# Kernel optimization log

Measured on AMD Instinct MI355X. Metric: run time of the kernel, lower is better.

Reference implementation:

```python
import jax, jax.numpy as jnp
import numpy as np

INPUT_SIZE = 1
HIDDEN = 20


def setup_inputs() -> dict:
    key = jax.random.key(0)
    ks = jax.random.split(key, 7)
    B, S = 4096, 512
    scale = 1.0 / np.sqrt(HIDDEN)  # torch LSTM/Linear init range
    x = jax.random.normal(ks[0], (B, S, INPUT_SIZE), dtype=jnp.float32)
    W_ih = jax.random.uniform(ks[1], (4 * HIDDEN, INPUT_SIZE), jnp.float32, -scale, scale)
    W_hh = jax.random.uniform(ks[2], (4 * HIDDEN, HIDDEN), jnp.float32, -scale, scale)
    b_ih = jax.random.uniform(ks[3], (4 * HIDDEN,), jnp.float32, -scale, scale)
    b_hh = jax.random.uniform(ks[4], (4 * HIDDEN,), jnp.float32, -scale, scale)
    W_lin = jax.random.uniform(ks[5], (1, HIDDEN), jnp.float32, -scale, scale)
    b_lin = jax.random.uniform(ks[6], (1,), jnp.float32, -scale, scale)
    return {"x": x, "W_ih": W_ih, "W_hh": W_hh, "b_ih": b_ih,
            "b_hh": b_hh, "W_lin": W_lin, "b_lin": b_lin}


def _lstm_seq(x, W_ih, W_hh, b_ih, b_hh):
    # x: [B, S, 1]; returns all hidden states [B, S, H]
    B = x.shape[0]
    # precompute input contribution for all timesteps: [S, B, 4H]
    xg = jnp.einsum('bsi,gi->sbg', x, W_ih) + (b_ih + b_hh)
    h0 = jnp.zeros((B, HIDDEN), x.dtype)
    c0 = jnp.zeros((B, HIDDEN), x.dtype)

    def step(carry, xg_t):
        h, c = carry
        gates = xg_t + h @ W_hh.T  # [B, 4H]
        i, f, g, o = jnp.split(gates, 4, axis=-1)  # torch gate order: i,f,g,o
        i = jax.nn.sigmoid(i)
        f = jax.nn.sigmoid(f)
        g = jnp.tanh(g)
        o = jax.nn.sigmoid(o)
        c_new = f * c + i * g
        h_new = o * jnp.tanh(c_new)
        return (h_new, c_new), h_new

    _, hs = jax.lax.scan(step, (h0, c0), xg)  # hs: [S, B, H]
    return jnp.transpose(hs, (1, 0, 2))  # [B, S, H]


def reference(x, W_ih, W_hh, b_ih, b_hh, W_lin, b_lin):
    h = _lstm_seq(x, W_ih, W_hh, b_ih, b_hh)  # [B, S, H]
    return h @ W_lin.T + b_lin  # [B, S, 1]
```

## Files before the change

kernel.cpp:

```cpp
#include <hip/hip_runtime.h>


#define BATCH 4096
#define SLEN  512
#define H     20
#define LOG2E 1.44269504088896340736f

typedef _Float16 f16x8 __attribute__((ext_vector_type(8)));
typedef _Float16 h2    __attribute__((ext_vector_type(2)));
typedef float    f32x4 __attribute__((ext_vector_type(4)));

__device__ __forceinline__ float fexp2(float x) { return __builtin_amdgcn_exp2f(x); }
__device__ __forceinline__ float frcp(float x)  { return __builtin_amdgcn_rcpf(x); }

#define ACT(Cv, CC, HV) {                                             \
    const float eI = fexp2((Cv)[0]);                                  \
    const float eF = fexp2((Cv)[1]);                                  \
    const float eG = fexp2((Cv)[2]);                                  \
    const float eO = fexp2((Cv)[3]);                                  \
    const float pF = 1.0f + eF;                                       \
    const float P  = (1.0f + eI) * (1.0f + eG);                       \
    const float num = fmaf(CC, P, (1.0f - eG) * pF);                  \
    CC = fmaxf(num * frcp(pF * P), -34.0f);                           \
    const float eC = fexp2(s2 * CC);                                  \
    HV = (1.0f - eC) * frcp((1.0f + eO) * (1.0f + eC));               \
}

__global__ __launch_bounds__(256, 1) void lstm_fused(
    const float* __restrict__ x,
    const float* __restrict__ W_ih,
    const float* __restrict__ W_hh,
    const float* __restrict__ b_ih,
    const float* __restrict__ b_hh,
    const float* __restrict__ W_lin,
    const float* __restrict__ b_lin,
    float* __restrict__ out)
{
    __shared__ __align__(16) _Float16 hrow[2][16][40];

    const int tid  = threadIdx.x;
    const int wv   = tid >> 6;
    const int lane = tid & 63;
    const int q    = lane >> 4;
    const int n    = lane & 15;
    const long b   = (long)blockIdx.x * 16 + n;

    const float s1 = -LOG2E;
    const float s2 = -2.0f * LOG2E;

    const int  m0   = (wv == 0) ? 0 : (wv + 1);
    const bool dual = (wv == 0);

    const int gA = n & 3;
    const int uA = (n >> 2) * 5;
    const float scA = (gA == 2) ? s2 : s1;
    f16x8 am0, am1;
    {
        const int r0 = gA * H + uA + m0;
        const int r1 = gA * H + uA + 1;
#pragma unroll
        for (int s = 0; s < 8; ++s) {
            am0[s] = (_Float16)((s < 5) ? scA * W_hh[r0 * H + 5 * q + s] : 0.0f);
            am1[s] = (_Float16)((s < 5) ? scA * W_hh[r1 * H + 5 * q + s] : 0.0f);
        }
    }
    f16x8 ah;
#pragma unroll
    for (int s = 0; s < 8; ++s)
        ah[s] = (_Float16)((n == 0 && s < 5) ? W_lin[5 * q + s] : 0.0f);
    const f32x4 chi = {(q == 0) ? b_lin[0] : 0.0f, 0.0f, 0.0f, 0.0f};

    f32x4 xw0, bb0, xw1, bb1;
#pragma unroll
    for (int r = 0; r < 4; ++r) {
        const float sc = (r == 2) ? s2 : s1;
        const int r0 = r * H + 5 * q + m0;
        const int r1 = r * H + 5 * q + 1;
        xw0[r] = sc * W_ih[r0];  bb0[r] = sc * (b_ih[r0] + b_hh[r0]);
        xw1[r] = sc * W_ih[r1];  bb1[r] = sc * (b_ih[r1] + b_hh[r1]);
    }

    const float* xb = x + b * SLEN;
    float*       ob = out + b * SLEN;

    for (int i = tid; i < 640; i += 256) ((unsigned*)hrow)[i] = 0u;
    __syncthreads();

    float cc0 = 0.0f, cc1 = 0.0f;
    f32x4 ya;
    f32x4 xc = *(const f32x4*)xb;

#define STEP(p)                                                            \
    {                                                                      \
        const f16x8 bf = *(const f16x8*)&hrow[((p) & 1) ^ 1][n][8 * q];    \
        if (wv == 3) {                                                     \
            const f32x4 Ch =                                               \
                __builtin_amdgcn_mfma_f32_16x16x32_f16(ah, bf, chi, 0, 0, 0); \
            const float yv = Ch[0];                  \
            if ((p) == 0) {                                                \
                ya[3] = yv;                                                \
                if (k > 0 && lane < 16) *(f32x4*)(ob + 4 * k - 4) = ya;    \
            } else if ((p) == 1) ya[0] = yv;                               \
            else if ((p) == 2) ya[1] = yv;                                 \
            else ya[2] = yv;                                               \
        }                                                                  \
        const float xt = xc[(p)];                                          \
        f32x4 ci0;                                                         \
        ci0[0] = fmaf(xt, xw0[0], bb0[0]);                                 \
        ci0[1] = fmaf(xt, xw0[1], bb0[1]);                                 \
        ci0[2] = fmaf(xt, xw0[2], bb0[2]);                                 \
        ci0[3] = fmaf(xt, xw0[3], bb0[3]);                                 \
        f32x4 C0 = __builtin_amdgcn_mfma_f32_16x16x32_f16(am0, bf, ci0, 0, 0, 0); \
        float h0v;                                                         \
        ACT(C0, cc0, h0v);                                                 \
        if (dual) {                                                        \
            f32x4 ci1;                                                     \
            ci1[0] = fmaf(xt, xw1[0], bb1[0]);                             \
            ci1[1] = fmaf(xt, xw1[1], bb1[1]);                             \
            ci1[2] = fmaf(xt, xw1[2], bb1[2]);                             \
            ci1[3] = fmaf(xt, xw1[3], bb1[3]);                             \
            f32x4 C1 = __builtin_amdgcn_mfma_f32_16x16x32_f16(am1, bf, ci1, 0, 0, 0); \
            float h1v;                                                     \
            ACT(C1, cc1, h1v);                                             \
            h2 pr; pr.x = (_Float16)h0v; pr.y = (_Float16)h1v;             \
            *(h2*)&hrow[(p) & 1][n][8 * q] = pr;          \
        } else {                                                           \
            hrow[(p) & 1][n][8 * q + m0] = (_Float16)h0v;                  \
        }                                                                  \
        __syncthreads();                                                   \
    }

#pragma unroll 1
    for (int k = 0; k < 128; ++k) {
        const int t0 = 4 * k;
        const int tn = (t0 + 4 < SLEN) ? t0 + 4 : SLEN - 4;
        const f32x4 xn = *(const f32x4*)(xb + tn);

        STEP(0) STEP(1) STEP(2) STEP(3)

        xc = xn;
    }
#undef STEP

    if (wv == 3) {
        const f16x8 bf = *(const f16x8*)&hrow[1][n][8 * q];
        const f32x4 Ch = __builtin_amdgcn_mfma_f32_16x16x32_f16(ah, bf, chi, 0, 0, 0);
        ya[3] = Ch[0];
        if (lane < 16) *(f32x4*)(ob + SLEN - 4) = ya;
    }
}

extern "C" void kernel_launch(void* const* d_in, const int* in_sizes, int n_in,
                              void* d_out, int out_size, void* d_ws, size_t ws_size,
                              hipStream_t stream) {
    const float* x     = (const float*)d_in[0];
    const float* W_ih  = (const float*)d_in[1];
    const float* W_hh  = (const float*)d_in[2];
    const float* b_ih  = (const float*)d_in[3];
    const float* b_hh  = (const float*)d_in[4];
    const float* W_lin = (const float*)d_in[5];
    const float* b_lin = (const float*)d_in[6];
    float* out = (float*)d_out;

    const int nblocks = BATCH / 16;
    lstm_fused<<<nblocks, 256, 0, stream>>>(x, W_ih, W_hh, b_ih, b_hh,
                                            W_lin, b_lin, out);
}
```

Measured before the change: 220.1 us.

## Halve batch per block to double grid size and rotate wave roles

Each block now handles 8 batch rows instead of 16, doubling the number of blocks so that all CUs (and two blocks per CU via launch bounds) get work on the serial recurrence. The upper 8 MFMA columns compute duplicate or unused rows and skip their stores. Wave roles are rotated by block index to spread the heavier dual-MFMA wave across SIMDs. The LDS row stride is padded to 44 halves with split 8-byte loads, aiming to reduce bank conflicts. Half the MFMA throughput is wasted on padding rows in exchange.

```diff
diff --git a/kernel.cpp b/kernel.cpp
--- a/kernel.cpp
+++ b/kernel.cpp
@@ -4,9 +4,12 @@
 #define BATCH 4096
 #define SLEN  512
 #define H     20
+#define CH    8
+#define RS    44
 #define LOG2E 1.44269504088896340736f
 
 typedef _Float16 f16x8 __attribute__((ext_vector_type(8)));
+typedef _Float16 f16x4 __attribute__((ext_vector_type(4)));
 typedef _Float16 h2    __attribute__((ext_vector_type(2)));
 typedef float    f32x4 __attribute__((ext_vector_type(4)));
 
@@ -26,7 +29,7 @@
     HV = (1.0f - eC) * frcp((1.0f + eO) * (1.0f + eC));               \
 }
 
-__global__ __launch_bounds__(256, 1) void lstm_fused(
+__global__ __launch_bounds__(256, 2) void lstm_fused(
     const float* __restrict__ x,
     const float* __restrict__ W_ih,
     const float* __restrict__ W_hh,
@@ -36,20 +39,22 @@
     const float* __restrict__ b_lin,
     float* __restrict__ out)
 {
-    __shared__ __align__(16) _Float16 hrow[2][16][40];
+    __shared__ __align__(16) _Float16 hrow[2][16][RS];
 
     const int tid  = threadIdx.x;
     const int wv   = tid >> 6;
     const int lane = tid & 63;
     const int q    = lane >> 4;
     const int n    = lane & 15;
-    const long b   = (long)blockIdx.x * 16 + n;
+    const bool nv  = (n < CH);
+    const long b   = (long)blockIdx.x * CH + (n & 7);
 
     const float s1 = -LOG2E;
     const float s2 = -2.0f * LOG2E;
 
-    const int  m0   = (wv == 0) ? 0 : (wv + 1);
-    const bool dual = (wv == 0);
+    const int  wr   = (wv + ((blockIdx.x ^ (blockIdx.x >> 8)) & 3)) & 3;
+    const int  m0   = (wr == 0) ? 0 : (wr + 1);
+    const bool dual = (wr == 0);
 
     const int gA = n & 3;
     const int uA = (n >> 2) * 5;
@@ -83,7 +88,7 @@
     const float* xb = x + b * SLEN;
     float*       ob = out + b * SLEN;
 
-    for (int i = tid; i < 640; i += 256) ((unsigned*)hrow)[i] = 0u;
+    for (int i = tid; i < 2 * 16 * RS / 2; i += 256) ((unsigned*)hrow)[i] = 0u;
     __syncthreads();
 
     float cc0 = 0.0f, cc1 = 0.0f;
@@ -92,14 +97,18 @@
 
 #define STEP(p)                                                            \
     {                                                                      \
-        const f16x8 bf = *(const f16x8*)&hrow[((p) & 1) ^ 1][n][8 * q];    \
-        if (wv == 3) {                                                     \
+        const _Float16* hp_ = &hrow[((p) & 1) ^ 1][n][8 * q];              \
+        const f16x4 lo_ = *(const f16x4*)hp_;                              \
+        const f16x4 hi_ = *(const f16x4*)(hp_ + 4);                        \
+        const f16x8 bf = __builtin_shufflevector(lo_, hi_,                 \
+                                                 0, 1, 2, 3, 4, 5, 6, 7); \
+        if (wr == 3) {                                                     \
             const f32x4 Ch =                                               \
                 __builtin_amdgcn_mfma_f32_16x16x32_f16(ah, bf, chi, 0, 0, 0); \
             const float yv = Ch[0];                  \
             if ((p) == 0) {                                                \
                 ya[3] = yv;                                                \
-                if (k > 0 && lane < 16) *(f32x4*)(ob + 4 * k - 4) = ya;    \
+                if (k > 0 && lane < CH) *(f32x4*)(ob + 4 * k - 4) = ya;    \
             } else if ((p) == 1) ya[0] = yv;                               \
             else if ((p) == 2) ya[1] = yv;                                 \
             else ya[2] = yv;                                               \
@@ -122,9 +131,11 @@
             f32x4 C1 = __builtin_amdgcn_mfma_f32_16x16x32_f16(am1, bf, ci1, 0, 0, 0); \
             float h1v;                                                     \
             ACT(C1, cc1, h1v);                                             \
-            h2 pr; pr.x = (_Float16)h0v; pr.y = (_Float16)h1v;             \
-            *(h2*)&hrow[(p) & 1][n][8 * q] = pr;          \
-        } else {                                                           \
+            if (nv) {                                                      \
+                h2 pr_; pr_.x = (_Float16)h0v; pr_.y = (_Float16)h1v;      \
+                *(h2*)&hrow[(p) & 1][n][8 * q] = pr_;     \
+            }                                                              \
+        } else if (nv) {                                                   \
             hrow[(p) & 1][n][8 * q + m0] = (_Float16)h0v;                  \
         }                                                                  \
         __syncthreads();                                                   \
@@ -142,11 +153,14 @@
     }
 #undef STEP
 
-    if (wv == 3) {
-        const f16x8 bf = *(const f16x8*)&hrow[1][n][8 * q];
+    if (wr == 3) {
+        const _Float16* hp_ = &hrow[1][n][8 * q];
+        const f16x4 lo_ = *(const f16x4*)hp_;
+        const f16x4 hi_ = *(const f16x4*)(hp_ + 4);
+        const f16x8 bf = __builtin_shufflevector(lo_, hi_, 0, 1, 2, 3, 4, 5, 6, 7);
         const f32x4 Ch = __builtin_amdgcn_mfma_f32_16x16x32_f16(ah, bf, chi, 0, 0, 0);
         ya[3] = Ch[0];
-        if (lane < 16) *(f32x4*)(ob + SLEN - 4) = ya;
+        if (lane < CH) *(f32x4*)(ob + SLEN - 4) = ya;
     }
 }
 
@@ -162,7 +176,7 @@
     const float* b_lin = (const float*)d_in[6];
     float* out = (float*)d_out;
 
-    const int nblocks = BATCH / 16;
+    const int nblocks = BATCH / CH;
     lstm_fused<<<nblocks, 256, 0, stream>>>(x, W_ih, W_hh, b_ih, b_hh,
                                             W_lin, b_lin, out);
 }
```

Measured after the change: 252.5 us. 1.15x slower.

## Split gate work across five waves plus a dedicated output-head wave

Applied to the files above, without the earlier changes.

Raises the block from 4 to 6 waves. Five waves each compute one hidden unit per group with a single MFMA and activation, replacing the old layout where wave 0 handled two units. A sixth wave computes only the linear output head. The hidden-state row stride becomes 44, so the 8-wide LDS read is split into two 4-wide reads. This shortens the per-step critical path of the slowest wave, at the cost of more threads taking part in every barrier.

```diff
diff --git a/kernel.cpp b/kernel.cpp
--- a/kernel.cpp
+++ b/kernel.cpp
@@ -4,10 +4,11 @@
 #define BATCH 4096
 #define SLEN  512
 #define H     20
+#define RS    44
 #define LOG2E 1.44269504088896340736f
 
 typedef _Float16 f16x8 __attribute__((ext_vector_type(8)));
-typedef _Float16 h2    __attribute__((ext_vector_type(2)));
+typedef _Float16 f16x4 __attribute__((ext_vector_type(4)));
 typedef float    f32x4 __attribute__((ext_vector_type(4)));
 
 __device__ __forceinline__ float fexp2(float x) { return __builtin_amdgcn_exp2f(x); }
@@ -26,7 +27,7 @@
     HV = (1.0f - eC) * frcp((1.0f + eO) * (1.0f + eC));               \
 }
 
-__global__ __launch_bounds__(256, 1) void lstm_fused(
+__global__ __launch_bounds__(384, 1) void lstm_fused(
     const float* __restrict__ x,
     const float* __restrict__ W_ih,
     const float* __restrict__ W_hh,
@@ -36,7 +37,7 @@
     const float* __restrict__ b_lin,
     float* __restrict__ out)
 {
-    __shared__ __align__(16) _Float16 hrow[2][16][40];
+    __shared__ __align__(16) _Float16 hrow[2][16][RS];
 
     const int tid  = threadIdx.x;
     const int wv   = tid >> 6;
@@ -48,21 +49,19 @@
     const float s1 = -LOG2E;
     const float s2 = -2.0f * LOG2E;
 
-    const int  m0   = (wv == 0) ? 0 : (wv + 1);
-    const bool dual = (wv == 0);
+    const bool isgate = (wv < 5);
+    const bool ishead = (wv == 5);
+    const int  m     = isgate ? wv : 0;
 
     const int gA = n & 3;
     const int uA = (n >> 2) * 5;
     const float scA = (gA == 2) ? s2 : s1;
-    f16x8 am0, am1;
+    f16x8 am;
     {
-        const int r0 = gA * H + uA + m0;
-        const int r1 = gA * H + uA + 1;
+        const int row = gA * H + uA + m;
 #pragma unroll
-        for (int s = 0; s < 8; ++s) {
-            am0[s] = (_Float16)((s < 5) ? scA * W_hh[r0 * H + 5 * q + s] : 0.0f);
-            am1[s] = (_Float16)((s < 5) ? scA * W_hh[r1 * H + 5 * q + s] : 0.0f);
-        }
+        for (int s = 0; s < 8; ++s)
+            am[s] = (_Float16)((s < 5) ? scA * W_hh[row * H + 5 * q + s] : 0.0f);
     }
     f16x8 ah;
 #pragma unroll
@@ -70,30 +69,35 @@
         ah[s] = (_Float16)((n == 0 && s < 5) ? W_lin[5 * q + s] : 0.0f);
     const f32x4 chi = {(q == 0) ? b_lin[0] : 0.0f, 0.0f, 0.0f, 0.0f};
 
-    f32x4 xw0, bb0, xw1, bb1;
+    f32x4 xw, bb;
 #pragma unroll
     for (int r = 0; r < 4; ++r) {
         const float sc = (r == 2) ? s2 : s1;
-        const int r0 = r * H + 5 * q + m0;
-        const int r1 = r * H + 5 * q + 1;
-        xw0[r] = sc * W_ih[r0];  bb0[r] = sc * (b_ih[r0] + b_hh[r0]);
-        xw1[r] = sc * W_ih[r1];  bb1[r] = sc * (b_ih[r1] + b_hh[r1]);
+        const int row = r * H + 5 * q + m;
+        xw[r] = sc * W_ih[row];
+        bb[r] = sc * (b_ih[row] + b_hh[row]);
     }
 
     const float* xb = x + b * SLEN;
     float*       ob = out + b * SLEN;
 
-    for (int i = tid; i < 640; i += 256) ((unsigned*)hrow)[i] = 0u;
+    for (int i = tid; i < 2 * 16 * RS / 2; i += 384) ((unsigned*)hrow)[i] = 0u;
     __syncthreads();
 
-    float cc0 = 0.0f, cc1 = 0.0f;
+    float cc = 0.0f;
     f32x4 ya;
     f32x4 xc = *(const f32x4*)xb;
 
 #define STEP(p)                                                            \
     {                                                                      \
-        const f16x8 bf = *(const f16x8*)&hrow[((p) & 1) ^ 1][n][8 * q];    \
-        if (wv == 3) {                                                     \
+        f16x8 bf;                                                          \
+        {                                                                  \
+            const _Float16* hp_ = &hrow[((p) & 1) ^ 1][n][8 * q];          \
+            const f16x4 lo_ = *(const f16x4*)hp_;                          \
+            const f16x4 hi_ = *(const f16x4*)(hp_ + 4);                    \
+            bf = __builtin_shufflevector(lo_, hi_, 0, 1, 2, 3, 4, 5, 6, 7); \
+        }                                                                  \
+        if (ishead) {                                                      \
             const f32x4 Ch =                                               \
                 __builtin_amdgcn_mfma_f32_16x16x32_f16(ah, bf, chi, 0, 0, 0); \
             const float yv = Ch[0];                  \
@@ -104,28 +108,17 @@
             else if ((p) == 2) ya[1] = yv;                                 \
             else ya[2] = yv;                                               \
         }                                                                  \
-        const float xt = xc[(p)];                                          \
-        f32x4 ci0;                                                         \
-        ci0[0] = fmaf(xt, xw0[0], bb0[0]);                                 \
-        ci0[1] = fmaf(xt, xw0[1], bb0[1]);                                 \
-        ci0[2] = fmaf(xt, xw0[2], bb0[2]);                                 \
-        ci0[3] = fmaf(xt, xw0[3], bb0[3]);                                 \
-        f32x4 C0 = __builtin_amdgcn_mfma_f32_16x16x32_f16(am0, bf, ci0, 0, 0, 0); \
-        float h0v;                                                         \
-        ACT(C0, cc0, h0v);                                                 \
-        if (dual) {                                                        \
-            f32x4 ci1;                                                     \
-            ci1[0] = fmaf(xt, xw1[0], bb1[0]);                             \
-            ci1[1] = fmaf(xt, xw1[1], bb1[1]);                             \
-            ci1[2] = fmaf(xt, xw1[2], bb1[2]);                             \
-            ci1[3] = fmaf(xt, xw1[3], bb1[3]);                             \
-            f32x4 C1 = __builtin_amdgcn_mfma_f32_16x16x32_f16(am1, bf, ci1, 0, 0, 0); \
-            float h1v;                                                     \
-            ACT(C1, cc1, h1v);                                             \
-            h2 pr; pr.x = (_Float16)h0v; pr.y = (_Float16)h1v;             \
-            *(h2*)&hrow[(p) & 1][n][8 * q] = pr;          \
-        } else {                                                           \
-            hrow[(p) & 1][n][8 * q + m0] = (_Float16)h0v;                  \
+        if (isgate) {                                                      \
+            const float xt = xc[(p)];                                      \
+            f32x4 ci;                                                      \
+            ci[0] = fmaf(xt, xw[0], bb[0]);                                \
+            ci[1] = fmaf(xt, xw[1], bb[1]);                                \
+            ci[2] = fmaf(xt, xw[2], bb[2]);                                \
+            ci[3] = fmaf(xt, xw[3], bb[3]);                                \
+            f32x4 C0 = __builtin_amdgcn_mfma_f32_16x16x32_f16(am, bf, ci, 0, 0, 0); \
+            float hv;                                                      \
+            ACT(C0, cc, hv);                                               \
+            hrow[(p) & 1][n][8 * q + m] = (_Float16)hv;                    \
         }                                                                  \
         __syncthreads();                                                   \
     }
@@ -142,8 +135,11 @@
     }
 #undef STEP
 
-    if (wv == 3) {
-        const f16x8 bf = *(const f16x8*)&hrow[1][n][8 * q];
+    if (ishead) {
+        const _Float16* hp_ = &hrow[1][n][8 * q];
+        const f16x4 lo_ = *(const f16x4*)hp_;
+        const f16x4 hi_ = *(const f16x4*)(hp_ + 4);
+        const f16x8 bf = __builtin_shufflevector(lo_, hi_, 0, 1, 2, 3, 4, 5, 6, 7);
         const f32x4 Ch = __builtin_amdgcn_mfma_f32_16x16x32_f16(ah, bf, chi, 0, 0, 0);
         ya[3] = Ch[0];
         if (lane < 16) *(f32x4*)(ob + SLEN - 4) = ya;
@@ -163,6 +159,6 @@
     float* out = (float*)d_out;
 
     const int nblocks = BATCH / 16;
-    lstm_fused<<<nblocks, 256, 0, stream>>>(x, W_ih, W_hh, b_ih, b_hh,
+    lstm_fused<<<nblocks, 384, 0, stream>>>(x, W_ih, W_hh, b_ih, b_hh,
                                             W_lin, b_lin, out);
 }
```

Measured after the change: 182.1 us. 17.3% less time.
